# Optimization experiments

Hardware: AMD Instinct MI355X
Metric: run time of the kernel (lower is better)

## Reference

```python
import jax, jax.numpy as jnp
import numpy as np

B = 256
D_MODEL = 2048
D_STATE = 128
D_CONV = 4
EXPAND = 2
HEADDIM = 64
D_INNER = EXPAND * D_MODEL          # 4096
NHEADS = D_INNER // HEADDIM         # 64
CONV_DIM = D_INNER + 2 * D_STATE    # 4352
D_IN_PROJ = 2 * D_INNER + 2 * D_STATE + NHEADS  # 8512
EPS = 1e-5


def setup_inputs() -> dict:
    key = jax.random.key(0)
    ks = jax.random.split(key, 10)
    rn = lambda k, shp, s=1.0: jax.random.normal(k, shp, jnp.float32) * s
    # dt_bias initialized like the torch module: inverse-softplus of dt ~ U[log 1e-3, log 1e-1]
    u = jax.random.uniform(ks[5], (NHEADS,), jnp.float32)
    dt = jnp.exp(u * (np.log(0.1) - np.log(0.001)) + np.log(0.001))
    dt = jnp.clip(dt, 1e-4, None)
    dt_bias = dt + jnp.log(-jnp.expm1(-dt))
    A_log = jnp.log(jax.random.uniform(ks[6], (NHEADS,), jnp.float32, minval=1.0, maxval=1.1))
    return {
        "hidden_states": rn(ks[0], (B, 1, D_MODEL)),
        "conv_state": rn(ks[1], (B, CONV_DIM, D_CONV)),
        "ssm_state": rn(ks[2], (B, NHEADS, HEADDIM, D_STATE), 0.1),
        "W_in": rn(ks[3], (D_IN_PROJ, D_MODEL), 0.02),
        "conv_w": rn(ks[4], (CONV_DIM, D_CONV), 0.1),  # conv1d.weight 'd 1 w' squeezed
        "conv_b": jnp.zeros((CONV_DIM,), jnp.float32),
        "dt_bias": dt_bias,
        "A_log": A_log,
        "D": jnp.ones((NHEADS,), jnp.float32),
        "norm_w": jnp.ones((D_INNER,), jnp.float32),
        "W_out": rn(ks[7], (D_MODEL, D_INNER), 0.02),
    }


def reference(hidden_states, conv_state, ssm_state, W_in, conv_w, conv_b,
              dt_bias, A_log, D, norm_w, W_out):
    h = hidden_states[:, 0, :]                    # [B, d_model]
    zxbcdt = h @ W_in.T                           # [B, d_in_proj]; d_mlp = 0
    z = zxbcdt[:, :D_INNER]
    xBC = zxbcdt[:, D_INNER:D_INNER + CONV_DIM]
    dt = zxbcdt[:, D_INNER + CONV_DIM:]           # [B, nheads]

    # roll conv buffer, append new token, depthwise conv over window
    cs = jnp.concatenate([conv_state[:, :, 1:], xBC[:, :, None]], axis=-1)  # [B, conv_dim, d_conv]
    xBC = jnp.sum(cs * conv_w[None, :, :], axis=-1) + conv_b
    xBC = jax.nn.silu(xBC)

    x = xBC[:, :D_INNER]
    Bm = xBC[:, D_INNER:D_INNER + D_STATE]        # [B, d_state]
    C = xBC[:, D_INNER + D_STATE:]                # [B, d_state]

    A = -jnp.exp(A_log)                           # [nheads]
    dt = jax.nn.softplus(dt + dt_bias)            # [B, nheads]
    dA = jnp.exp(dt * A)                          # [B, nheads]

    xh = x.reshape(B, NHEADS, HEADDIM)            # [B, h, p]
    dBx = jnp.einsum('bh,bn,bhp->bhpn', dt, Bm, xh)
    ss = ssm_state * dA[:, :, None, None] + dBx   # [B, h, p, n]
    y = jnp.einsum('bhpn,bn->bhp', ss, C) + D[None, :, None] * xh
    y = y.reshape(B, D_INNER)

    # gated RMSNorm (gate before norm, single group)
    y = y * jax.nn.silu(z)
    y = y * jax.lax.rsqrt(jnp.mean(y * y, axis=-1, keepdims=True) + EPS) * norm_w

    out = y @ W_out.T                             # [B, d_model]
    return out[:, None, :]
```

## Files before the change

### kernel.cpp

```cpp
#include <hip/hip_runtime.h>
#include <hip/hip_bf16.h>
#include <math.h>

#define BATCH     256
#define DMODEL    2048
#define DSTATE    128
#define HEADDIM_  64
#define DINNER    4096
#define NHEADS_   64
#define CONVDIM   4352
#define DINPROJ   8512
#define EPS_      1e-5f

typedef __attribute__((ext_vector_type(8))) short short8;
typedef __attribute__((ext_vector_type(4))) short short4v;
typedef __attribute__((ext_vector_type(4))) float f32x4;

__device__ __forceinline__ short bfbits(float f) {
    __hip_bfloat16 h = __float2bfloat16(f);
    return *reinterpret_cast<short*>(&h);
}
__device__ __forceinline__ short8 cvt8(float4 a, float4 b) {
    short8 r;
    r[0] = bfbits(a.x); r[1] = bfbits(a.y); r[2] = bfbits(a.z); r[3] = bfbits(a.w);
    r[4] = bfbits(b.x); r[5] = bfbits(b.y); r[6] = bfbits(b.z); r[7] = bfbits(b.w);
    return r;
}
__device__ __forceinline__ int swz(int row, int cb) {
    return row * 128 + (cb ^ ((row & 7) << 4));
}

__global__ __launch_bounds__(256)
void f2b(const float* __restrict__ in, short* __restrict__ o) {
    int i = (blockIdx.x * 256 + threadIdx.x) * 8;
    float4 a = *(const float4*)(in + i);
    float4 b = *(const float4*)(in + i + 4);
    *(short8*)(o + i) = cvt8(a, b);
}

template<int TH, int BN>
__global__ __launch_bounds__(TH, 2)
void gemm_mfma(const short* __restrict__ A, const float* __restrict__ W,
               float* __restrict__ C, int lda, int ldb, int ldc, int kc) {
    constexpr int NW  = TH / 64;
    constexpr int WNC = BN / 32;
    constexpr int ASL = 2048 / TH;
    constexpr int BBYTES = BN * 128;
    const int bn0 = blockIdx.x * BN;
    const int k0  = blockIdx.z * kc;
    C += (size_t)blockIdx.z * 256 * ldc;
    const int t = threadIdx.x;
    const int lane = t & 63;
    const int w = t >> 6;
    const int wm = w / WNC, wn = w % WNC;
    const int fr = lane & 15, fg = lane >> 4;

    __shared__ __align__(16) char lds[2][32768 + BBYTES];

    const short* apb[ASL]; int ao[ASL];
    #pragma unroll
    for (int i = 0; i < ASL; ++i) {
        int s = t + TH * i, r = s >> 3, sl = s & 7;
        apb[i] = A + (size_t)r * lda + k0 + sl * 8;
        ao[i] = swz(r, sl * 16);
    }
    const int br = t >> 3, bsl = t & 7;
    const float* bp = W + (size_t)(bn0 + br) * ldb + k0 + bsl * 8;
    const int bo = 32768 + swz(br, bsl * 16);

    int aro[4], bro[2];
    #pragma unroll
    for (int m = 0; m < 4; ++m) aro[m] = swz(wm * 64 + m * 16 + fr, fg * 16);
    #pragma unroll
    for (int n = 0; n < 2; ++n) bro[n] = 32768 + swz(wn * 32 + n * 16 + fr, fg * 16);

    f32x4 acc[4][2] = {};
    short8 rab[ASL];
    float4 rb0, rb1;

    #define LOADT(kt) { const int ko = (kt) << 6;                                \
        _Pragma("unroll") for (int i = 0; i < ASL; ++i)                          \
            rab[i] = *(const short8*)(apb[i] + ko);                              \
        rb0 = *(const float4*)(bp + ko); rb1 = *(const float4*)(bp + ko + 4); }
    #define STAGET(buf) {                                                        \
        _Pragma("unroll") for (int i = 0; i < ASL; ++i)                          \
            *(short8*)(lds[buf] + ao[i]) = rab[i];                               \
        *(short8*)(lds[buf] + bo) = cvt8(rb0, rb1); }

    LOADT(0);
    STAGET(0);
    int cur = 0;
    const int nT = kc >> 6;
    for (int kt = 0; kt < nT; ++kt) {
        if (kt + 1 < nT) LOADT(kt + 1);
        __syncthreads();
        #pragma unroll
        for (int ks = 0; ks < 2; ++ks) {
            short8 af[4], bf[2];
            #pragma unroll
            for (int m = 0; m < 4; ++m) af[m] = *(short8*)(lds[cur] + (aro[m] ^ (ks << 6)));
            #pragma unroll
            for (int n = 0; n < 2; ++n) bf[n] = *(short8*)(lds[cur] + (bro[n] ^ (ks << 6)));
            #pragma unroll
            for (int m = 0; m < 4; ++m)
                #pragma unroll
                for (int n = 0; n < 2; ++n)
                    acc[m][n] = __builtin_amdgcn_mfma_f32_16x16x32_bf16(af[m], bf[n], acc[m][n], 0, 0, 0);
        }
        if (kt + 1 < nT) STAGET(cur ^ 1);
        cur ^= 1;
    }
    #pragma unroll
    for (int m = 0; m < 4; ++m)
        #pragma unroll
        for (int n = 0; n < 2; ++n) {
            const int row = wm * 64 + m * 16 + fg * 4;
            const int col = bn0 + wn * 32 + n * 16 + fr;
            #pragma unroll
            for (int j = 0; j < 4; ++j)
                C[(size_t)(row + j) * ldc + col] = acc[m][n][j];
        }
    #undef LOADT
    #undef STAGET
}

__global__ __launch_bounds__(256)
void reduce4(const float* __restrict__ part, float* __restrict__ out) {
    const int i = (blockIdx.x * 256 + threadIdx.x) * 4;
    float4 s = *(const float4*)(part + i);
    #pragma unroll
    for (int k = 1; k < 4; ++k) {
        float4 p = *(const float4*)(part + (size_t)k * BATCH * DMODEL + i);
        s.x += p.x; s.y += p.y; s.z += p.z; s.w += p.w;
    }
    *(float4*)(out + i) = s;
}

__global__ __launch_bounds__(1024)
void fused_mid(const float* __restrict__ zx, const float* __restrict__ conv_state,
               const float* __restrict__ conv_w, const float* __restrict__ conv_b,
               const float* __restrict__ dt_bias, const float* __restrict__ A_log,
               const float* __restrict__ ssm, const float* __restrict__ Dp,
               const float* __restrict__ nw, short* __restrict__ yn) {
    const int b = blockIdx.x, t = threadIdx.x;
    const int lane = t & 63, w = t >> 6;
    __shared__ float sxbc[CONVDIM];
    __shared__ float sy[DINNER];
    __shared__ float sred[16];
    __shared__ float sdA[NHEADS_], scoef[NHEADS_];

    #pragma unroll
    for (int it = 0; it < 5; ++it) {
        int c = it * 1024 + t;
        if (c < CONVDIM) {
            float4 cs = *(const float4*)&conv_state[((size_t)b * CONVDIM + c) * 4];
            float4 w4 = *(const float4*)&conv_w[c * 4];
            float xin = zx[(size_t)b * DINPROJ + DINNER + c];
            float v = cs.y * w4.x + cs.z * w4.y + cs.w * w4.z + xin * w4.w + conv_b[c];
            sxbc[c] = v / (1.f + expf(-v));
        }
    }
    __syncthreads();

    if (t < 128) {
        float prod = sxbc[DINNER + t] * sxbc[DINNER + DSTATE + t];
        #pragma unroll
        for (int m = 1; m < 64; m <<= 1) prod += __shfl_xor(prod, m);
        if ((t & 63) == 0) sred[t >> 6] = prod;
    }
    __syncthreads();
    if (t < NHEADS_) {
        float BC = sred[0] + sred[1];
        float x = zx[(size_t)b * DINPROJ + DINNER + CONVDIM + t] + dt_bias[t];
        float dt = (x > 20.f) ? x : log1pf(expf(x));
        sdA[t] = expf(dt * (-expf(A_log[t])));
        scoef[t] = dt * BC + Dp[t];
    }
    __syncthreads();

    {
        const int pq = lane >> 4, nl = lane & 15;
        const float4 c4a = *(const float4*)&sxbc[DINNER + DSTATE + nl * 8];
        const float4 c4b = *(const float4*)&sxbc[DINNER + DSTATE + nl * 8 + 4];
        #pragma unroll
        for (int k = 0; k < 4; ++k) {
            const int h = w * 4 + k;
            const float* S = ssm + (((size_t)b * NHEADS_ + h) * HEADDIM_) * DSTATE;
            const float dA = sdA[h], coef = scoef[h];
            #pragma unroll 4
            for (int pp = 0; pp < 16; ++pp) {
                const int p = pp * 4 + pq;
                float4 sa = *(const float4*)&S[p * DSTATE + nl * 8];
                float4 sb = *(const float4*)&S[p * DSTATE + nl * 8 + 4];
                float dot = sa.x * c4a.x + sa.y * c4a.y + sa.z * c4a.z + sa.w * c4a.w
                          + sb.x * c4b.x + sb.y * c4b.y + sb.z * c4b.z + sb.w * c4b.w;
                #pragma unroll
                for (int m = 1; m < 16; m <<= 1) dot += __shfl_xor(dot, m);
                if (nl == 0)
                    sy[h * HEADDIM_ + p] = dA * dot + sxbc[h * HEADDIM_ + p] * coef;
            }
        }
    }
    __syncthreads();

    {
        const int i = t * 4;
        float4 yv = *(const float4*)&sy[i];
        float4 zv = *(const float4*)&zx[(size_t)b * DINPROJ + i];
        float4 g;
        g.x = yv.x * (zv.x / (1.f + expf(-zv.x)));
        g.y = yv.y * (zv.y / (1.f + expf(-zv.y)));
        g.z = yv.z * (zv.z / (1.f + expf(-zv.z)));
        g.w = yv.w * (zv.w / (1.f + expf(-zv.w)));
        float ss = g.x * g.x + g.y * g.y + g.z * g.z + g.w * g.w;
        #pragma unroll
        for (int m = 1; m < 64; m <<= 1) ss += __shfl_xor(ss, m);
        __syncthreads();
        if (lane == 0) sred[w] = ss;
        __syncthreads();
        float tot = 0.f;
        #pragma unroll
        for (int k = 0; k < 16; ++k) tot += sred[k];
        const float sc = rsqrtf(tot * (1.f / DINNER) + EPS_);
        float4 w4 = *(const float4*)&nw[i];
        short4v o;
        o[0] = bfbits(g.x * sc * w4.x); o[1] = bfbits(g.y * sc * w4.y);
        o[2] = bfbits(g.z * sc * w4.z); o[3] = bfbits(g.w * sc * w4.w);
        *(short4v*)&yn[(size_t)b * DINNER + i] = o;
    }
}

extern "C" void kernel_launch(void* const* d_in, const int* in_sizes, int n_in,
                              void* d_out, int out_size, void* d_ws, size_t ws_size,
                              hipStream_t stream) {
    const float* hid        = (const float*)d_in[0];
    const float* conv_state = (const float*)d_in[1];
    const float* ssm        = (const float*)d_in[2];
    const float* W_in       = (const float*)d_in[3];
    const float* conv_w     = (const float*)d_in[4];
    const float* conv_b     = (const float*)d_in[5];
    const float* dt_bias    = (const float*)d_in[6];
    const float* A_log      = (const float*)d_in[7];
    const float* Dp         = (const float*)d_in[8];
    const float* norm_w     = (const float*)d_in[9];
    const float* W_out      = (const float*)d_in[10];
    float* out = (float*)d_out;

    float* ws    = (float*)d_ws;
    float* zx    = ws;
    float* part  = zx + (size_t)BATCH * DINPROJ;
    short* hidbf = (short*)(part + (size_t)4 * BATCH * DMODEL);
    short* yn_bf = hidbf + (size_t)BATCH * DMODEL;

    f2b<<<dim3(BATCH * DMODEL / 2048), 256, 0, stream>>>(hid, hidbf);
    gemm_mfma<512, 64><<<dim3(DINPROJ / 64, 1, 1), 512, 0, stream>>>(
        hidbf, W_in, zx, DMODEL, DMODEL, DINPROJ, DMODEL);
    fused_mid<<<dim3(BATCH), 1024, 0, stream>>>(
        zx, conv_state, conv_w, conv_b, dt_bias, A_log, ssm, Dp, norm_w, yn_bf);
    gemm_mfma<256, 32><<<dim3(DMODEL / 32, 1, 4), 256, 0, stream>>>(
        yn_bf, W_out, part, DINNER, DINNER, DMODEL, DINNER / 4);
    reduce4<<<dim3(BATCH * DMODEL / 1024), 256, 0, stream>>>(part, out);
}
```

Before: 181.4 us.

## Read A fragments directly from global, use atomic split-K for out-projection

The GEMM now loads the bf16 activation fragments straight from global memory into registers instead of staging them through LDS, and stages only the converted weight tile with a 128-wide K step. The out-projection switches to an 8-way split-K over 512-thread blocks that accumulates into a zeroed output with atomic adds, which removes the partial buffer and the separate reduce kernel. The SSM loop unroll is also raised. This trades LDS traffic and an extra kernel for redundant global A reads across waves, atomic contention, and a memset, and the atomic summation order is non-deterministic.

```diff
diff --git a/kernel.cpp b/kernel.cpp
--- a/kernel.cpp
+++ b/kernel.cpp
@@ -26,9 +26,6 @@
     r[4] = bfbits(b.x); r[5] = bfbits(b.y); r[6] = bfbits(b.z); r[7] = bfbits(b.w);
     return r;
 }
-__device__ __forceinline__ int swz(int row, int cb) {
-    return row * 128 + (cb ^ ((row & 7) << 4));
-}
 
 __global__ __launch_bounds__(256)
 void f2b(const float* __restrict__ in, short* __restrict__ o) {
@@ -38,76 +35,76 @@
     *(short8*)(o + i) = cvt8(a, b);
 }
 
-template<int TH, int BN>
-__global__ __launch_bounds__(TH, 2)
+template<bool ATOMIC>
+__global__ __launch_bounds__(512, 2)
 void gemm_mfma(const short* __restrict__ A, const float* __restrict__ W,
                float* __restrict__ C, int lda, int ldb, int ldc, int kc) {
-    constexpr int NW  = TH / 64;
-    constexpr int WNC = BN / 32;
-    constexpr int ASL = 2048 / TH;
-    constexpr int BBYTES = BN * 128;
-    const int bn0 = blockIdx.x * BN;
+    const int bn0 = blockIdx.x * 64;
     const int k0  = blockIdx.z * kc;
-    C += (size_t)blockIdx.z * 256 * ldc;
     const int t = threadIdx.x;
     const int lane = t & 63;
     const int w = t >> 6;
-    const int wm = w / WNC, wn = w % WNC;
+    const int wm = w >> 1, wn = w & 1;
     const int fr = lane & 15, fg = lane >> 4;
 
-    __shared__ __align__(16) char lds[2][32768 + BBYTES];
-
-    const short* apb[ASL]; int ao[ASL];
-    #pragma unroll
-    for (int i = 0; i < ASL; ++i) {
-        int s = t + TH * i, r = s >> 3, sl = s & 7;
-        apb[i] = A + (size_t)r * lda + k0 + sl * 8;
-        ao[i] = swz(r, sl * 16);
-    }
-    const int br = t >> 3, bsl = t & 7;
-    const float* bp = W + (size_t)(bn0 + br) * ldb + k0 + bsl * 8;
-    const int bo = 32768 + swz(br, bsl * 16);
-
-    int aro[4], bro[2];
-    #pragma unroll
-    for (int m = 0; m < 4; ++m) aro[m] = swz(wm * 64 + m * 16 + fr, fg * 16);
-    #pragma unroll
-    for (int n = 0; n < 2; ++n) bro[n] = 32768 + swz(wn * 32 + n * 16 + fr, fg * 16);
+    __shared__ __align__(16) char lds[2][16384];
+
+    const float* bp[2]; int bo[2];
+    #pragma unroll
+    for (int i = 0; i < 2; ++i) {
+        int s = t + 512 * i, r = s >> 4, sl = s & 15;
+        bp[i] = W + (size_t)(bn0 + r) * ldb + k0 + sl * 8;
+        bo[i] = r * 256 + ((sl * 16) ^ ((r & 15) << 4));
+    }
+    int brbase[2], brmask[2];
+    #pragma unroll
+    for (int n = 0; n < 2; ++n) {
+        int row = wn * 32 + n * 16 + fr;
+        brbase[n] = row * 256;
+        brmask[n] = (row & 15) << 4;
+    }
+    const short* Afp[4];
+    #pragma unroll
+    for (int m = 0; m < 4; ++m)
+        Afp[m] = A + (size_t)(wm * 64 + m * 16 + fr) * lda + k0 + fg * 8;
 
     f32x4 acc[4][2] = {};
-    short8 rab[ASL];
-    float4 rb0, rb1;
-
-    #define LOADT(kt) { const int ko = (kt) << 6;                                \
-        _Pragma("unroll") for (int i = 0; i < ASL; ++i)                          \
-            rab[i] = *(const short8*)(apb[i] + ko);                              \
-        rb0 = *(const float4*)(bp + ko); rb1 = *(const float4*)(bp + ko + 4); }
-    #define STAGET(buf) {                                                        \
-        _Pragma("unroll") for (int i = 0; i < ASL; ++i)                          \
-            *(short8*)(lds[buf] + ao[i]) = rab[i];                               \
-        *(short8*)(lds[buf] + bo) = cvt8(rb0, rb1); }
-
-    LOADT(0);
-    STAGET(0);
+    float4 rb[2][2];
+
+    #define LOADB(kt) { const int ko = (kt) << 7;                                  \
+        _Pragma("unroll") for (int i = 0; i < 2; ++i) {                            \
+            rb[i][0] = *(const float4*)(bp[i] + ko);                               \
+            rb[i][1] = *(const float4*)(bp[i] + ko + 4); } }
+    #define STAGEB(buf) {                                                          \
+        _Pragma("unroll") for (int i = 0; i < 2; ++i)                              \
+            *(short8*)(lds[buf] + bo[i]) = cvt8(rb[i][0], rb[i][1]); }
+
+    LOADB(0);
+    STAGEB(0);
     int cur = 0;
-    const int nT = kc >> 6;
+    const int nT = kc >> 7;
     for (int kt = 0; kt < nT; ++kt) {
-        if (kt + 1 < nT) LOADT(kt + 1);
         __syncthreads();
-        #pragma unroll
-        for (int ks = 0; ks < 2; ++ks) {
-            short8 af[4], bf[2];
-            #pragma unroll
-            for (int m = 0; m < 4; ++m) af[m] = *(short8*)(lds[cur] + (aro[m] ^ (ks << 6)));
-            #pragma unroll
-            for (int n = 0; n < 2; ++n) bf[n] = *(short8*)(lds[cur] + (bro[n] ^ (ks << 6)));
+        short8 af[4][4];
+        #pragma unroll
+        for (int m = 0; m < 4; ++m)
+            #pragma unroll
+            for (int ks = 0; ks < 4; ++ks)
+                af[m][ks] = *(const short8*)(Afp[m] + (kt << 7) + ks * 32);
+        if (kt + 1 < nT) LOADB(kt + 1);
+        #pragma unroll
+        for (int ks = 0; ks < 4; ++ks) {
+            short8 bf[2];
+            #pragma unroll
+            for (int n = 0; n < 2; ++n)
+                bf[n] = *(short8*)(lds[cur] + brbase[n] + ((ks * 64 + fg * 16) ^ brmask[n]));
             #pragma unroll
             for (int m = 0; m < 4; ++m)
                 #pragma unroll
                 for (int n = 0; n < 2; ++n)
-                    acc[m][n] = __builtin_amdgcn_mfma_f32_16x16x32_bf16(af[m], bf[n], acc[m][n], 0, 0, 0);
-        }
-        if (kt + 1 < nT) STAGET(cur ^ 1);
+                    acc[m][n] = __builtin_amdgcn_mfma_f32_16x16x32_bf16(af[m][ks], bf[n], acc[m][n], 0, 0, 0);
+        }
+        if (kt + 1 < nT) STAGEB(cur ^ 1);
         cur ^= 1;
     }
     #pragma unroll
@@ -117,23 +114,15 @@
             const int row = wm * 64 + m * 16 + fg * 4;
             const int col = bn0 + wn * 32 + n * 16 + fr;
             #pragma unroll
-            for (int j = 0; j < 4; ++j)
-                C[(size_t)(row + j) * ldc + col] = acc[m][n][j];
-        }
-    #undef LOADT
-    #undef STAGET
-}
-
-__global__ __launch_bounds__(256)
-void reduce4(const float* __restrict__ part, float* __restrict__ out) {
-    const int i = (blockIdx.x * 256 + threadIdx.x) * 4;
-    float4 s = *(const float4*)(part + i);
-    #pragma unroll
-    for (int k = 1; k < 4; ++k) {
-        float4 p = *(const float4*)(part + (size_t)k * BATCH * DMODEL + i);
-        s.x += p.x; s.y += p.y; s.z += p.z; s.w += p.w;
-    }
-    *(float4*)(out + i) = s;
+            for (int j = 0; j < 4; ++j) {
+                if (ATOMIC)
+                    unsafeAtomicAdd(&C[(size_t)(row + j) * ldc + col], acc[m][n][j]);
+                else
+                    C[(size_t)(row + j) * ldc + col] = acc[m][n][j];
+            }
+        }
+    #undef LOADB
+    #undef STAGEB
 }
 
 __global__ __launch_bounds__(1024)
@@ -187,7 +176,7 @@
             const int h = w * 4 + k;
             const float* S = ssm + (((size_t)b * NHEADS_ + h) * HEADDIM_) * DSTATE;
             const float dA = sdA[h], coef = scoef[h];
-            #pragma unroll 4
+            #pragma unroll 8
             for (int pp = 0; pp < 16; ++pp) {
                 const int p = pp * 4 + pq;
                 float4 sa = *(const float4*)&S[p * DSTATE + nl * 8];
@@ -248,16 +237,15 @@
 
     float* ws    = (float*)d_ws;
     float* zx    = ws;
-    float* part  = zx + (size_t)BATCH * DINPROJ;
-    short* hidbf = (short*)(part + (size_t)4 * BATCH * DMODEL);
+    short* hidbf = (short*)(zx + (size_t)BATCH * DINPROJ);
     short* yn_bf = hidbf + (size_t)BATCH * DMODEL;
 
+    hipMemsetAsync(d_out, 0, (size_t)out_size * sizeof(float), stream);
     f2b<<<dim3(BATCH * DMODEL / 2048), 256, 0, stream>>>(hid, hidbf);
-    gemm_mfma<512, 64><<<dim3(DINPROJ / 64, 1, 1), 512, 0, stream>>>(
+    gemm_mfma<false><<<dim3(DINPROJ / 64, 1, 1), 512, 0, stream>>>(
         hidbf, W_in, zx, DMODEL, DMODEL, DINPROJ, DMODEL);
     fused_mid<<<dim3(BATCH), 1024, 0, stream>>>(
         zx, conv_state, conv_w, conv_b, dt_bias, A_log, ssm, Dp, norm_w, yn_bf);
-    gemm_mfma<256, 32><<<dim3(DMODEL / 32, 1, 4), 256, 0, stream>>>(
-        yn_bf, W_out, part, DINNER, DINNER, DMODEL, DINNER / 4);
-    reduce4<<<dim3(BATCH * DMODEL / 1024), 256, 0, stream>>>(part, out);
-}
+    gemm_mfma<true><<<dim3(DMODEL / 64, 1, 8), 512, 0, stream>>>(
+        yn_bf, W_out, out, DINNER, DINNER, DMODEL, DINNER / 8);
+}
```

Result: slower. 237.0 us (+30.6%).

## Split-K the input projection GEMM in two, sum partials in fused kernel

Applied to the files above, without the earlier changes.

The input projection GEMM gains a split-K factor of two, doubling its grid from 133 to 266 blocks so more of the GPU's compute units get work. The two partial results are summed inside fused_mid wherever z, xBC and dt are read, so no separate reduction kernel is needed. The SSM state loop also uses nontemporal loads and unrolls 8 instead of 4. In exchange it writes and reads twice the intermediate data (an extra 256x8512 float buffer).

```diff
diff --git a/kernel.cpp b/kernel.cpp
--- a/kernel.cpp
+++ b/kernel.cpp
@@ -42,7 +42,6 @@
 __global__ __launch_bounds__(TH, 2)
 void gemm_mfma(const short* __restrict__ A, const float* __restrict__ W,
                float* __restrict__ C, int lda, int ldb, int ldc, int kc) {
-    constexpr int NW  = TH / 64;
     constexpr int WNC = BN / 32;
     constexpr int ASL = 2048 / TH;
     constexpr int BBYTES = BN * 128;
@@ -137,7 +136,8 @@
 }
 
 __global__ __launch_bounds__(1024)
-void fused_mid(const float* __restrict__ zx, const float* __restrict__ conv_state,
+void fused_mid(const float* __restrict__ zp0, const float* __restrict__ zp1,
+               const float* __restrict__ conv_state,
                const float* __restrict__ conv_w, const float* __restrict__ conv_b,
                const float* __restrict__ dt_bias, const float* __restrict__ A_log,
                const float* __restrict__ ssm, const float* __restrict__ Dp,
@@ -155,7 +155,8 @@
         if (c < CONVDIM) {
             float4 cs = *(const float4*)&conv_state[((size_t)b * CONVDIM + c) * 4];
             float4 w4 = *(const float4*)&conv_w[c * 4];
-            float xin = zx[(size_t)b * DINPROJ + DINNER + c];
+            float xin = zp0[(size_t)b * DINPROJ + DINNER + c]
+                      + zp1[(size_t)b * DINPROJ + DINNER + c];
             float v = cs.y * w4.x + cs.z * w4.y + cs.w * w4.z + xin * w4.w + conv_b[c];
             sxbc[c] = v / (1.f + expf(-v));
         }
@@ -171,7 +172,8 @@
     __syncthreads();
     if (t < NHEADS_) {
         float BC = sred[0] + sred[1];
-        float x = zx[(size_t)b * DINPROJ + DINNER + CONVDIM + t] + dt_bias[t];
+        float x = zp0[(size_t)b * DINPROJ + DINNER + CONVDIM + t]
+                + zp1[(size_t)b * DINPROJ + DINNER + CONVDIM + t] + dt_bias[t];
         float dt = (x > 20.f) ? x : log1pf(expf(x));
         sdA[t] = expf(dt * (-expf(A_log[t])));
         scoef[t] = dt * BC + Dp[t];
@@ -187,13 +189,13 @@
             const int h = w * 4 + k;
             const float* S = ssm + (((size_t)b * NHEADS_ + h) * HEADDIM_) * DSTATE;
             const float dA = sdA[h], coef = scoef[h];
-            #pragma unroll 4
+            #pragma unroll 8
             for (int pp = 0; pp < 16; ++pp) {
                 const int p = pp * 4 + pq;
-                float4 sa = *(const float4*)&S[p * DSTATE + nl * 8];
-                float4 sb = *(const float4*)&S[p * DSTATE + nl * 8 + 4];
-                float dot = sa.x * c4a.x + sa.y * c4a.y + sa.z * c4a.z + sa.w * c4a.w
-                          + sb.x * c4b.x + sb.y * c4b.y + sb.z * c4b.z + sb.w * c4b.w;
+                f32x4 sa = __builtin_nontemporal_load((const f32x4*)&S[p * DSTATE + nl * 8]);
+                f32x4 sb = __builtin_nontemporal_load((const f32x4*)&S[p * DSTATE + nl * 8 + 4]);
+                float dot = sa[0] * c4a.x + sa[1] * c4a.y + sa[2] * c4a.z + sa[3] * c4a.w
+                          + sb[0] * c4b.x + sb[1] * c4b.y + sb[2] * c4b.z + sb[3] * c4b.w;
                 #pragma unroll
                 for (int m = 1; m < 16; m <<= 1) dot += __shfl_xor(dot, m);
                 if (nl == 0)
@@ -206,7 +208,9 @@
     {
         const int i = t * 4;
         float4 yv = *(const float4*)&sy[i];
-        float4 zv = *(const float4*)&zx[(size_t)b * DINPROJ + i];
+        float4 z0 = *(const float4*)&zp0[(size_t)b * DINPROJ + i];
+        float4 z1 = *(const float4*)&zp1[(size_t)b * DINPROJ + i];
+        float4 zv = { z0.x + z1.x, z0.y + z1.y, z0.z + z1.z, z0.w + z1.w };
         float4 g;
         g.x = yv.x * (zv.x / (1.f + expf(-zv.x)));
         g.y = yv.y * (zv.y / (1.f + expf(-zv.y)));
@@ -247,16 +251,17 @@
     float* out = (float*)d_out;
 
     float* ws    = (float*)d_ws;
-    float* zx    = ws;
-    float* part  = zx + (size_t)BATCH * DINPROJ;
+    float* zpart = ws;
+    float* part  = zpart + (size_t)2 * BATCH * DINPROJ;
     short* hidbf = (short*)(part + (size_t)4 * BATCH * DMODEL);
     short* yn_bf = hidbf + (size_t)BATCH * DMODEL;
 
     f2b<<<dim3(BATCH * DMODEL / 2048), 256, 0, stream>>>(hid, hidbf);
-    gemm_mfma<512, 64><<<dim3(DINPROJ / 64, 1, 1), 512, 0, stream>>>(
-        hidbf, W_in, zx, DMODEL, DMODEL, DINPROJ, DMODEL);
+    gemm_mfma<512, 64><<<dim3(DINPROJ / 64, 1, 2), 512, 0, stream>>>(
+        hidbf, W_in, zpart, DMODEL, DMODEL, DINPROJ, DMODEL / 2);
     fused_mid<<<dim3(BATCH), 1024, 0, stream>>>(
-        zx, conv_state, conv_w, conv_b, dt_bias, A_log, ssm, Dp, norm_w, yn_bf);
+        zpart, zpart + (size_t)BATCH * DINPROJ,
+        conv_state, conv_w, conv_b, dt_bias, A_log, ssm, Dp, norm_w, yn_bf);
     gemm_mfma<256, 32><<<dim3(DMODEL / 32, 1, 4), 256, 0, stream>>>(
         yn_bf, W_out, part, DINNER, DINNER, DMODEL, DINNER / 4);
     reduce4<<<dim3(BATCH * DMODEL / 1024), 256, 0, stream>>>(part, out);
```

Measured after the change: 148.4 us. -18.2%, faster.
